# Kernel optimization log

Measured on AMD Instinct MI355X. Metric: run time of the kernel, lower is better.

Reference implementation:

```python
import jax, jax.numpy as jnp
import numpy as np
from jax.scipy.special import logsumexp

G, H, L, N, K = 2000, 128, 10, 4096, 10
TAU, LC, LA, EPS = 0.1, 1.0, 0.5, 1e-6

def _lin_init(k, fi, fo):
    return jax.random.normal(k, (fi, fo), jnp.float32) / np.sqrt(fi)

def setup_inputs():
    key = jax.random.key(0)
    ks = jax.random.split(key, 12)
    return {
        'wt_x': jax.random.normal(ks[0], (N, G), jnp.float32),
        'ko_x': jax.random.normal(ks[1], (N, G), jnp.float32),
        'wt_labels': jax.random.randint(ks[2], (N,), 0, K, dtype=jnp.int32),
        'ko_labels': jax.random.randint(ks[3], (N,), 0, K, dtype=jnp.int32),
        'enc_w1': _lin_init(ks[4], G, H), 'enc_b1': jnp.zeros((H,)),
        'enc_g': jnp.ones((H,)), 'enc_be': jnp.zeros((H,)),
        'enc_w2': _lin_init(ks[5], H, L), 'enc_b2': jnp.zeros((L,)),
        'kap_w1': _lin_init(ks[6], G, H), 'kap_b1': jnp.zeros((H,)),
        'kap_g': jnp.ones((H,)), 'kap_be': jnp.zeros((H,)),
        'kap_w2': _lin_init(ks[7], H, 1), 'kap_b2': jnp.zeros((1,)),
        'dec_w1': _lin_init(ks[8], L, H), 'dec_b1': jnp.zeros((H,)),
        'dec_g': jnp.ones((H,)), 'dec_be': jnp.zeros((H,)),
        'dec_w2': _lin_init(ks[9], H, G), 'dec_b2': jnp.zeros((G,)),
    }

def _mlp(x, w1, b1, g, be, w2, b2):
    # Linear -> LayerNorm -> ReLU -> Linear (dropout_prob=0)
    h = x @ w1 + b1
    m = h.mean(-1, keepdims=True)
    v = ((h - m) ** 2).mean(-1, keepdims=True)
    h = (h - m) / jnp.sqrt(v + 1e-5) * g + be
    return jax.nn.relu(h) @ w2 + b2

def _contrastive(z_wt, z_ko, y_wt, y_ko):
    S = (z_wt @ z_ko.T) / TAU  # [Nwt, Nko], unit-norm z so |S| <= 1/tau
    total = jnp.float32(0.0)
    n_shared = jnp.float32(0.0)
    for c in range(K):  # fixed small class count
        mwt = (y_wt == c).astype(S.dtype)
        mko = (y_ko == c).astype(S.dtype)
        n_wt, n_ko = mwt.sum(), mko.sum()
        valid = (n_wt > 0) & (n_ko > 0)
        nw, nk = jnp.maximum(n_wt, 1.0), jnp.maximum(n_ko, 1.0)
        # mean_{i in c, j in c} (LSE_i - S_ij) over ko columns of class c
        lse_r = logsumexp(jnp.where(mko[None, :] > 0, S, -1e4), axis=1)
        l1 = jnp.sum(mwt * (lse_r - (S @ mko) / nk)) / nw
        lse_c = logsumexp(jnp.where(mwt[:, None] > 0, S, -1e4), axis=0)
        l2 = jnp.sum(mko * (lse_c - (mwt @ S) / nw)) / nk
        total = total + jnp.where(valid, 0.5 * (l1 + l2), 0.0)
        n_shared = n_shared + valid.astype(S.dtype)
    return jnp.where(n_shared > 0, total / jnp.maximum(n_shared, 1.0), 0.0)

def _alignment(z, y):
    ones = jnp.ones(z.shape[0], z.dtype)
    counts = jax.ops.segment_sum(ones, y, num_segments=K)
    mu_c = jax.ops.segment_sum(z, y, num_segments=K) / jnp.maximum(counts, 1.0)[:, None]
    dev = z - mu_c[y]
    per_class = jax.ops.segment_sum(jnp.sum(dev ** 2, axis=1), y, num_segments=K) / jnp.maximum(counts, 1.0)
    present = counts > 0
    return jnp.sum(jnp.where(present, per_class, 0.0)) / jnp.maximum(jnp.sum(present.astype(z.dtype)), 1.0)

def reference(wt_x, ko_x, enc_w1, enc_b1, enc_g, enc_be, enc_w2, enc_b2, kap_w1, kap_b1, kap_g, kap_be, kap_w2, kap_b2, dec_w1, dec_b1, dec_g, dec_be, dec_w2, dec_b2, wt_labels, ko_labels):
    def encode(x):
        mu = _mlp(x, enc_w1, enc_b1, enc_g, enc_be, enc_w2, enc_b2)
        mu = mu / jnp.maximum(jnp.linalg.norm(mu, axis=1, keepdims=True), 1e-12)
        kappa = jax.nn.softplus(_mlp(x, kap_w1, kap_b1, kap_g, kap_be, kap_w2, kap_b2)) + EPS
        return mu, kappa
    wt_mu, wt_kappa = encode(wt_x)
    ko_mu, ko_kappa = encode(ko_x)
    wt_z, ko_z = wt_mu, ko_mu  # eval mode: z = mu (deterministic)
    wt_rec = _mlp(wt_z, dec_w1, dec_b1, dec_g, dec_be, dec_w2, dec_b2)
    ko_rec = _mlp(ko_z, dec_w1, dec_b1, dec_g, dec_be, dec_w2, dec_b2)
    recon = jnp.mean((wt_rec - wt_x) ** 2) + jnp.mean((ko_rec - ko_x) ** 2)
    kl = (wt_kappa.mean() + ko_kappa.mean()) * 0.01
    contrast = _contrastive(wt_z, ko_z, wt_labels, ko_labels)
    align = _alignment(jnp.concatenate([wt_z, ko_z], 0), jnp.concatenate([wt_labels, ko_labels], 0))
    return recon + kl + LC * contrast + LA * align
```

## Files before the change

kernel.cpp:

```cpp
#include <hip/hip_runtime.h>
#include <math.h>

typedef __attribute__((ext_vector_type(8))) __bf16 bf16x8;
typedef __attribute__((ext_vector_type(4))) float f32x4;

#define GL2LDS_(gptr, lptr) \
    __builtin_amdgcn_global_load_lds((const __attribute__((address_space(1))) void*)(gptr), \
                                     (__attribute__((address_space(3))) void*)(lptr), 16, 0, 0)

#define OFF_NWT   0
#define OFF_NKO   10
#define OFF_L1    20
#define OFF_L2    30
#define OFF_REC   162
#define IOFF_WTOFF 192
#define IOFF_KOOFF 204
#define IOFF_WTCTR 216
#define ACC_FLOATS 256

#define WT_OFF    256
#define WTLO_OFF  (WT_OFF + 262144)
#define H_OFF     (WTLO_OFF + 262144)
#define Z_OFF     (H_OFF + 2097152)
#define KAP_OFF   (Z_OFF + 81920)
#define HREST_OFF (KAP_OFF + 8192)
#define HPART     2097152

__global__ __launch_bounds__(256) void pack_w_kernel(const float* __restrict__ enc_w1,
                                                     const float* __restrict__ kap_w1,
                                                     __bf16* __restrict__ WThi)
{
    __shared__ float tile[64][65];
    int kt = blockIdx.x & 31;
    int ct = blockIdx.x >> 5;
    int k0 = kt * 64, c0 = ct * 64;
    int t = threadIdx.x;
    int lr = t >> 6, lc = t & 63;
#pragma unroll
    for (int i = 0; i < 16; ++i) {
        int k = k0 + lr + 4 * i;
        int c = c0 + lc;
        float v = 0.f;
        if (k < 2000) v = (c < 128) ? enc_w1[(size_t)k * 128 + c]
                                    : kap_w1[(size_t)k * 128 + (c - 128)];
        tile[lc][lr + 4 * i] = v;
    }
    __syncthreads();
#pragma unroll
    for (int i = 0; i < 16; ++i) {
        int c = c0 + lr + 4 * i;
        int k = k0 + lc;
        WThi[(size_t)c * 2048 + k] = (__bf16)tile[lr + 4 * i][lc];
    }
}

__global__ __launch_bounds__(256) void pack_dw2_kernel(const float* __restrict__ dw2,
                                                       __bf16* __restrict__ BThi)
{
    __shared__ float tile[64][129];
    int j0 = blockIdx.x * 64;
    int t = threadIdx.x;
#pragma unroll
    for (int i = 0; i < 32; ++i) {
        int idx = i * 256 + t;
        int c = idx >> 6, jj = idx & 63;
        int j = j0 + jj;
        tile[jj][c] = (j < 2000) ? dw2[(size_t)c * 2000 + j] : 0.f;
    }
    __syncthreads();
#pragma unroll
    for (int i = 0; i < 32; ++i) {
        int idx = i * 256 + t;
        int jj = idx >> 7, c = idx & 127;
        BThi[(size_t)(j0 + jj) * 128 + c] = (__bf16)tile[jj][c];
    }
}

__global__ void counts_kernel(const int* __restrict__ wtl, const int* __restrict__ kol,
                              float* __restrict__ acc)
{
    __shared__ int cw[10], ck[10];
    int t = threadIdx.x;
    if (t < 10) { cw[t] = 0; ck[t] = 0; }
    __syncthreads();
    for (int i = t; i < 4096; i += 1024) {
        atomicAdd(&cw[wtl[i]], 1);
        atomicAdd(&ck[kol[i]], 1);
    }
    __syncthreads();
    if (t < 10) { acc[OFF_NWT + t] = (float)cw[t]; acc[OFF_NKO + t] = (float)ck[t]; }
    if (t == 0) {
        int* ai = (int*)acc;
        int aw = 0, ak = 0;
        for (int c = 0; c < 10; ++c) {
            ai[IOFF_WTOFF + c] = aw; aw += cw[c];
            ai[IOFF_KOOFF + c] = ak; ak += ck[c];
        }
        ai[IOFF_WTOFF + 10] = aw;
        ai[IOFF_KOOFF + 10] = ak;
    }
}

__global__ __launch_bounds__(512) void gemm1_kernel(const float* __restrict__ wt_x,
                                                    const float* __restrict__ ko_x,
                                                    const __bf16* __restrict__ WThi,
                                                    float* __restrict__ Hb,
                                                    float* __restrict__ Hrest,
                                                    int nkc)
{
    __shared__ short Bs[2][2][4096];
    int t = threadIdx.x;
    int widx = t >> 6, lane = t & 63;
    int wm = widx >> 1, wn = widx & 1;
    int b = blockIdx.x;
    int mt = b & 63, strip = (b >> 6) & 1, kc = b >> 7;
    int R0 = mt * 128;
    int cb = strip * 128;
    int kchunk = 2048 / nkc;
    int kbase = kc * kchunk;
    int kleft = 2000 - kbase;
    int nsteps = (kleft < kchunk) ? ((kleft + 31) >> 5) : (kchunk >> 5);
    int ntiles = (nsteps + 1) >> 1;

    const float* xb = (R0 < 4096) ? (wt_x + (size_t)R0 * 2000)
                                  : (ko_x + (size_t)(R0 - 4096) * 2000);
    int ar = wm * 32 + (lane & 15);
    const float* xrow0 = xb + (size_t)ar * 2000 + kbase;
    const float* xrow1 = xrow0 + (size_t)16 * 2000;
    int kboff = (lane >> 4) * 8;

    int col0 = t >> 2;
    int s0   = (t & 3) ^ ((col0 >> 1) & 3);
    size_t boff = (size_t)(cb + col0) * 2048 + kbase + s0 * 8;
    const __bf16* bsrcH = WThi + boff;

#define STAGEB_(buf, tl) do { \
    int st_ = (tl) * 2; \
    GL2LDS_(bsrcH + (size_t)st_ * 32,       &Bs[buf][0][t * 8]); \
    GL2LDS_(bsrcH + (size_t)(st_ + 1) * 32, &Bs[buf][1][t * 8]); } while (0)

    f32x4 acc00, acc01, acc02, acc03;
    f32x4 acc10, acc11, acc12, acc13;
#pragma unroll
    for (int r = 0; r < 4; ++r) {
        acc00[r]=0.f; acc01[r]=0.f; acc02[r]=0.f; acc03[r]=0.f;
        acc10[r]=0.f; acc11[r]=0.f; acc12[r]=0.f; acc13[r]=0.f;
    }

    float4 aA00, aA01, aA10, aA11, aA20, aA21, aA30, aA31;
    float4 aB00, aB01, aB10, aB11, aB20, aB21, aB30, aB31;

#define GLOADA_(step, a00, a01, a10, a11) do { \
    int k0_ = (step) * 32; \
    int k_ = k0_ + kboff; \
    if (kbase + k0_ <= 1952) { \
        a00 = *(const float4*)(xrow0 + k_); \
        a01 = *(const float4*)(xrow0 + k_ + 4); \
        a10 = *(const float4*)(xrow1 + k_); \
        a11 = *(const float4*)(xrow1 + k_ + 4); \
    } else { \
        float t0_[8], t1_[8]; \
        _Pragma("unroll") \
        for (int j = 0; j < 8; ++j) { \
            int kk = kbase + k_ + j; \
            t0_[j] = (kk < 2000) ? xrow0[k_ + j] : 0.f; \
            t1_[j] = (kk < 2000) ? xrow1[k_ + j] : 0.f; } \
        a00 = make_float4(t0_[0], t0_[1], t0_[2], t0_[3]); \
        a01 = make_float4(t0_[4], t0_[5], t0_[6], t0_[7]); \
        a10 = make_float4(t1_[0], t1_[1], t1_[2], t1_[3]); \
        a11 = make_float4(t1_[4], t1_[5], t1_[6], t1_[7]); } } while (0)

#define CONVH_(a0, a1, ahi) do { \
    float av_[8] = {a0.x, a0.y, a0.z, a0.w, a1.x, a1.y, a1.z, a1.w}; \
    _Pragma("unroll") \
    for (int j = 0; j < 8; ++j) ahi[j] = (__bf16)av_[j]; } while (0)

#define MFMAH_(buf, half, ahi0, ahi1) do { \
    _Pragma("unroll") \
    for (int nf = 0; nf < 4; ++nf) { \
        bf16x8 bhf = *(const bf16x8*)&Bs[buf][half][(ubase + nf * 64) * 8]; \
        f32x4* p0 = (nf == 0) ? &acc00 : (nf == 1) ? &acc01 : (nf == 2) ? &acc02 : &acc03; \
        f32x4* p1 = (nf == 0) ? &acc10 : (nf == 1) ? &acc11 : (nf == 2) ? &acc12 : &acc13; \
        *p0 = __builtin_amdgcn_mfma_f32_16x16x32_bf16(ahi0, bhf, *p0, 0, 0, 0); \
        *p1 = __builtin_amdgcn_mfma_f32_16x16x32_bf16(ahi1, bhf, *p1, 0, 0, 0); } } while (0)

    STAGEB_(0, 0);
    GLOADA_(0, aA00, aA01, aA10, aA11);
    GLOADA_(1, aA20, aA21, aA30, aA31);
    if (1 < ntiles) {
        GLOADA_(2, aB00, aB01, aB10, aB11);
        GLOADA_(3, aB20, aB21, aB30, aB31);
    }
    __syncthreads();

    int cpr = lane & 15;
    int pph = (lane >> 4) ^ ((cpr >> 1) & 3);
    int ubase = (wn * 64 + cpr) * 4 + pph;

    int half_iters = (ntiles + 1) >> 1;
    for (int it = 0; it < half_iters; ++it) {
        int tl = it * 2;
        {
            if (tl + 1 < ntiles) STAGEB_(1, tl + 1);
            bf16x8 h00, h01, h10, h11;
            CONVH_(aA00, aA01, h00); CONVH_(aA10, aA11, h01);
            CONVH_(aA20, aA21, h10); CONVH_(aA30, aA31, h11);
            if (tl + 2 < ntiles) {
                GLOADA_(2*(tl+2),   aA00, aA01, aA10, aA11);
                GLOADA_(2*(tl+2)+1, aA20, aA21, aA30, aA31);
            }
            MFMAH_(0, 0, h00, h01);
            MFMAH_(0, 1, h10, h11);
            __syncthreads();
        }
        if (tl + 1 < ntiles) {
            if (tl + 2 < ntiles) STAGEB_(0, tl + 2);
            bf16x8 h00, h01, h10, h11;
            CONVH_(aB00, aB01, h00); CONVH_(aB10, aB11, h01);
            CONVH_(aB20, aB21, h10); CONVH_(aB30, aB31, h11);
            if (tl + 3 < ntiles) {
                GLOADA_(2*(tl+3),   aB00, aB01, aB10, aB11);
                GLOADA_(2*(tl+3)+1, aB20, aB21, aB30, aB31);
            }
            MFMAH_(1, 0, h00, h01);
            MFMAH_(1, 1, h10, h11);
            __syncthreads();
        }
    }

    float* Hq = (kc == 0) ? Hb : (Hrest + (size_t)(kc - 1) * HPART);
#pragma unroll
    for (int r = 0; r < 4; ++r) {
        int row0 = R0 + wm * 32 + (lane >> 4) * 4 + r;
        size_t base0 = (size_t)row0 * 256 + cb + wn * 64 + (lane & 15);
        Hq[base0]      = acc00[r];
        Hq[base0 + 16] = acc01[r];
        Hq[base0 + 32] = acc02[r];
        Hq[base0 + 48] = acc03[r];
        size_t base1 = base0 + (size_t)16 * 256;
        Hq[base1]      = acc10[r];
        Hq[base1 + 16] = acc11[r];
        Hq[base1 + 32] = acc12[r];
        Hq[base1 + 48] = acc13[r];
    }
#undef STAGEB_
#undef GLOADA_
#undef CONVH_
#undef MFMAH_
}

__global__ __launch_bounds__(128) void stage2_kernel(const float* __restrict__ Hb,
    const float* __restrict__ Hrest, int nkc,
    const float* __restrict__ enc_b1, const float* __restrict__ enc_g, const float* __restrict__ enc_be,
    const float* __restrict__ enc_w2, const float* __restrict__ enc_b2,
    const float* __restrict__ kap_b1, const float* __restrict__ kap_g, const float* __restrict__ kap_be,
    const float* __restrict__ kap_w2, const float* __restrict__ kap_b2,
    const float* __restrict__ dw1, const float* __restrict__ db1,
    const float* __restrict__ dg,  const float* __restrict__ dbe,
    float* __restrict__ Z, float* __restrict__ Kap,
    __bf16* __restrict__ Ahi)
{
    __shared__ float sh[128];
    __shared__ float shz[10];
    __shared__ float dred[2], dvar[2];
    int row  = blockIdx.x;
    int wave = threadIdx.x >> 6;
    int lane = threadIdx.x & 63;
    size_t hoff = (size_t)row * 256 + wave * 128;
    const float* hb  = Hb + hoff;
    const float* b1 = wave ? kap_b1 : enc_b1;
    const float* gg = wave ? kap_g  : enc_g;
    const float* bb = wave ? kap_be : enc_be;

    float h0 = hb[lane]      + b1[lane];
    float h1 = hb[lane + 64] + b1[lane + 64];
    for (int j = 0; j + 1 < nkc; ++j) {
        const float* hr = Hrest + (size_t)j * HPART + hoff;
        h0 += hr[lane];
        h1 += hr[lane + 64];
    }
    float s = h0 + h1;
#pragma unroll
    for (int o = 32; o > 0; o >>= 1) s += __shfl_xor(s, o, 64);
    float m = s * (1.f / 128.f);
    float d0 = h0 - m, d1 = h1 - m;
    float v = d0 * d0 + d1 * d1;
#pragma unroll
    for (int o = 32; o > 0; o >>= 1) v += __shfl_xor(v, o, 64);
    v *= (1.f / 128.f);
    float sc = 1.f / sqrtf(v + 1e-5f);
    float r0 = fmaxf(fmaf(d0 * sc, gg[lane],      bb[lane]),      0.f);
    float r1 = fmaxf(fmaf(d1 * sc, gg[lane + 64], bb[lane + 64]), 0.f);

    if (wave == 0) { sh[lane] = r0; sh[lane + 64] = r1; }
    __syncthreads();

    if (wave == 0) {
        float mu = 0.f;
        if (lane < 10) {
            mu = enc_b2[lane];
            for (int c = 0; c < 128; ++c) mu = fmaf(sh[c], enc_w2[c * 10 + lane], mu);
        }
        float n2 = mu * mu;
#pragma unroll
        for (int o = 8; o > 0; o >>= 1) n2 += __shfl_xor(n2, o, 16);
        float inv = 1.f / fmaxf(sqrtf(n2), 1e-12f);
        if (lane < 10) {
            float zv = mu * inv;
            Z[(size_t)row * 10 + lane] = zv;
            shz[lane] = zv;
        }
    } else {
        float p = r0 * kap_w2[lane] + r1 * kap_w2[lane + 64];
#pragma unroll
        for (int o = 32; o > 0; o >>= 1) p += __shfl_xor(p, o, 64);
        if (lane == 0) {
            float x = p + kap_b2[0];
            float sp = (x > 20.f) ? x : log1pf(expf(x));
            Kap[row] = sp + 1e-6f;
        }
    }
    __syncthreads();

    {
        float z[10];
#pragma unroll
        for (int d = 0; d < 10; ++d) z[d] = shz[d];
        int c = threadIdx.x;
        float h = db1[c];
#pragma unroll
        for (int d = 0; d < 10; ++d) h = fmaf(z[d], dw1[d * 128 + c], h);
        float s2 = h;
#pragma unroll
        for (int o = 32; o > 0; o >>= 1) s2 += __shfl_xor(s2, o, 64);
        if (lane == 0) dred[wave] = s2;
        __syncthreads();
        float m2 = (dred[0] + dred[1]) * (1.f / 128.f);
        float dd = h - m2;
        float v2 = dd * dd;
#pragma unroll
        for (int o = 32; o > 0; o >>= 1) v2 += __shfl_xor(v2, o, 64);
        if (lane == 0) dvar[wave] = v2;
        __syncthreads();
        float var = (dvar[0] + dvar[1]) * (1.f / 128.f);
        float sc2 = 1.f / sqrtf(var + 1e-5f);
        float a = fmaxf(fmaf(dd * sc2, dg[c], dbe[c]), 0.f);
        Ahi[(size_t)row * 128 + c] = (__bf16)a;
    }
}

__global__ __launch_bounds__(256) void scatter_align_kernel(const float* __restrict__ Z,
                                                            const int* __restrict__ wtl,
                                                            const int* __restrict__ kol,
                                                            const float* __restrict__ Kap,
                                                            float* __restrict__ acc,
                                                            float* __restrict__ ZcWT,
                                                            float* __restrict__ ZcKO,
                                                            float* __restrict__ Part)
{
    __shared__ int lcnt[20];
    __shared__ int lbase[20];
    __shared__ float cL[10], qL[10], sL[100], ks;
    int t = threadIdx.x;
    if (t < 20) lcnt[t] = 0;
    if (t < 10) { cL[t] = 0.f; qL[t] = 0.f; }
    if (t >= 20 && t < 120) sL[t - 20] = 0.f;
    if (t == 120) ks = 0.f;
    __syncthreads();
    int row = blockIdx.x * 256 + t;
    int side = row >= 4096;
    int r = side ? row - 4096 : row;
    int c = side ? kol[r] : wtl[r];
    int key = side * 10 + c;
    int myrank = atomicAdd(&lcnt[key], 1);
    float zz[10]; float q = 0.f;
    const float* zr = Z + (size_t)row * 10;
#pragma unroll
    for (int d = 0; d < 10; ++d) { zz[d] = zr[d]; q = fmaf(zz[d], zz[d], q); }
    atomicAdd(&cL[c], 1.f);
    atomicAdd(&qL[c], q);
#pragma unroll
    for (int d = 0; d < 10; ++d) atomicAdd(&sL[c * 10 + d], zz[d]);
    atomicAdd(&ks, Kap[row]);
    __syncthreads();
    int* ai = (int*)acc;
    if (t < 20 && lcnt[t] > 0)
        lbase[t] = atomicAdd(&ai[IOFF_WTCTR + t], lcnt[t]);
    __syncthreads();
    int off = side ? ai[IOFF_KOOFF + c] : ai[IOFF_WTOFF + c];
    int slot = off + lbase[key] + myrank;
    float* dst = side ? ZcKO : ZcWT;
#pragma unroll
    for (int d = 0; d < 10; ++d) dst[d * 4096 + slot] = zz[d];
    float* pb = Part + (size_t)blockIdx.x * 128;
    if (t < 10)  { pb[t] = cL[t]; pb[10 + t] = qL[t]; }
    if (t < 100) pb[20 + t] = sL[t];
    if (t == 0)  pb[120] = ks;
}

__global__ __launch_bounds__(512, 4) void dec_gemm_kernel(
    const __bf16* __restrict__ Ahi,
    const __bf16* __restrict__ BThi,
    const float* __restrict__ wt_x, const float* __restrict__ ko_x,
    const float* __restrict__ db2, float* __restrict__ acc)
{
    __shared__ short BsH[2][8192];
    __shared__ float rs[8];
    int t = threadIdx.x;
    int widx = t >> 6, lane = t & 63;
    int wm = widx >> 2, wn = widx & 3;
    int R0 = (blockIdx.x >> 1) * 32;
    int T0 = (blockIdx.x & 1) * 16;
    const float* xbase = (R0 < 4096) ? wt_x : ko_x;
    int xr0 = ((R0 < 4096) ? R0 : R0 - 4096) + wm * 16 + (lane >> 4) * 4;

    size_t abase = (size_t)(R0 + wm * 16 + (lane & 15)) * 128 + (lane >> 4) * 8;
    bf16x8 ah0 = *(const bf16x8*)(Ahi + abase);
    bf16x8 ah1 = *(const bf16x8*)(Ahi + abase + 32);
    bf16x8 ah2 = *(const bf16x8*)(Ahi + abase + 64);
    bf16x8 ah3 = *(const bf16x8*)(Ahi + abase + 96);

    int g0c = t >> 4,         g0s = t & 15;
    int g1c = (t + 512) >> 4, g1s = t & 15;
    int u0 = g0c * 16 + (g0s ^ (g0c & 7));
    int u1 = g1c * 16 + (g1s ^ (g1c & 7));

    int col_local = wn * 16 + (lane & 15);
    int cl7 = col_local & 7;
    int rb = col_local * 16;
    int sb = lane >> 4;

    uint4 hA0, hA1, hB0, hB1;

#define GLOADB_(tile, h0, h1) do { \
    size_t gb = (size_t)(tile) * 8192; \
    h0 = *(const uint4*)(BThi + gb + (size_t)t * 8); \
    h1 = *(const uint4*)(BThi + gb + (size_t)(t + 512) * 8); } while (0)

#define DSWRITE_(buf, h0, h1) do { \
    *(uint4*)&BsH[buf][u0 * 8] = h0; \
    *(uint4*)&BsH[buf][u1 * 8] = h1; } while (0)

#define COMPUTE_(buf, tile) do { \
    int un0 = rb + ((sb +  0) ^ cl7); \
    int un1 = rb + ((sb +  4) ^ cl7); \
    int un2 = rb + ((sb +  8) ^ cl7); \
    int un3 = rb + ((sb + 12) ^ cl7); \
    bf16x8 bh0 = *(const bf16x8*)&BsH[buf][un0 * 8]; \
    bf16x8 bh1 = *(const bf16x8*)&BsH[buf][un1 * 8]; \
    bf16x8 bh2 = *(const bf16x8*)&BsH[buf][un2 * 8]; \
    bf16x8 bh3 = *(const bf16x8*)&BsH[buf][un3 * 8]; \
    f32x4 a4; \
    _Pragma("unroll") \
    for (int r = 0; r < 4; ++r) a4[r] = 0.f; \
    a4 = __builtin_amdgcn_mfma_f32_16x16x32_bf16(ah0, bh0, a4, 0, 0, 0); \
    a4 = __builtin_amdgcn_mfma_f32_16x16x32_bf16(ah1, bh1, a4, 0, 0, 0); \
    a4 = __builtin_amdgcn_mfma_f32_16x16x32_bf16(ah2, bh2, a4, 0, 0, 0); \
    a4 = __builtin_amdgcn_mfma_f32_16x16x32_bf16(ah3, bh3, a4, 0, 0, 0); \
    int col = (tile) * 64 + col_local; \
    if (col < 2000) { \
        float bb = db2[col]; \
        _Pragma("unroll") \
        for (int r = 0; r < 4; ++r) { \
            float xv = xbase[(size_t)(xr0 + r) * 2000 + col]; \
            float e = a4[r] + bb - xv; \
            rsum = fmaf(e, e, rsum); \
        } } } while (0)

    float rsum = 0.f;
    GLOADB_(T0 + 0, hA0, hA1);
    GLOADB_(T0 + 1, hB0, hB1);
    DSWRITE_(0, hA0, hA1);
    __syncthreads();

    for (int it = 0; it < 8; ++it) {
        int lt = it * 2;
        {
            if (lt + 2 < 16) GLOADB_(T0 + lt + 2, hA0, hA1);
            DSWRITE_(1, hB0, hB1);
            COMPUTE_(0, T0 + lt);
            __syncthreads();
        }
        {
            if (lt + 3 < 16) GLOADB_(T0 + lt + 3, hB0, hB1);
            if (lt + 2 < 16) DSWRITE_(0, hA0, hA1);
            COMPUTE_(1, T0 + lt + 1);
            __syncthreads();
        }
    }

#pragma unroll
    for (int o = 32; o > 0; o >>= 1) rsum += __shfl_xor(rsum, o, 64);
    if (lane == 0) rs[widx] = rsum;
    __syncthreads();
    if (t == 0) {
        float s = 0.f;
#pragma unroll
        for (int w = 0; w < 8; ++w) s += rs[w];
        atomicAdd(&acc[OFF_REC], s);
    }
#undef GLOADB_
#undef DSWRITE_
#undef COMPUTE_
}

#define MAXNB 768
__global__ __launch_bounds__(256) void contrast_kernel(const float* __restrict__ ZcWT,
                                                       const float* __restrict__ ZcKO,
                                                       float* __restrict__ acc)
{
    __shared__ float zb[MAXNB * 12];
    __shared__ float bsum[4];
    int b = blockIdx.x;
    int cs = b / 3, sub = b - cs * 3;
    int c = cs >> 1, side = cs & 1;
    const int* ai = (const int*)acc;
    int aStart = side ? ai[IOFF_KOOFF + c]     : ai[IOFF_WTOFF + c];
    int aEnd   = side ? ai[IOFF_KOOFF + c + 1] : ai[IOFF_WTOFF + c + 1];
    int bStart = side ? ai[IOFF_WTOFF + c]     : ai[IOFF_KOOFF + c];
    int bEnd   = side ? ai[IOFF_WTOFF + c + 1] : ai[IOFF_KOOFF + c + 1];
    int na = aEnd - aStart;
    int nb = bEnd - bStart;
    if (nb > MAXNB) nb = MAXNB;
    const float* ZA = side ? ZcKO : ZcWT;
    const float* ZB = side ? ZcWT : ZcKO;
    int t = threadIdx.x;

    for (int u = t; u < nb; u += 256) {
#pragma unroll
        for (int d = 0; d < 10; ++d) zb[u * 12 + d] = ZB[d * 4096 + bStart + u];
    }
    __syncthreads();

    int chunk = (na + 2) / 3;
    int r0 = sub * chunk;
    int rcnt = na - r0; if (rcnt > chunk) rcnt = chunk;

    float wsum = 0.f;
    bool waveActive = (nb > 0) && ((t & ~63) < rcnt);
    if (waveActive) {
        bool valid = t < rcnt;
        int ar = aStart + (valid ? (r0 + t) : 0);
        float za[10];
#pragma unroll
        for (int d = 0; d < 10; ++d) za[d] = ZA[d * 4096 + ar];
        float se = 0.f, ss = 0.f;
        for (int u = 0; u < nb; ++u) {
            const float* zp = &zb[u * 12];
            float s = 0.f;
#pragma unroll
            for (int d = 0; d < 10; ++d) s = fmaf(za[d], zp[d], s);
            s *= 10.f;
            se += __expf(s - 10.f);
            ss += s;
        }
        if (valid) wsum = (10.f + __logf(se)) - ss / (float)nb;
    }
#pragma unroll
    for (int o = 32; o > 0; o >>= 1) wsum += __shfl_xor(wsum, o, 64);
    if ((t & 63) == 0) bsum[t >> 6] = wsum;
    __syncthreads();
    if (t == 0) {
        float s = bsum[0] + bsum[1] + bsum[2] + bsum[3];
        if (s != 0.f || nb > 0)
            atomicAdd(&acc[(side ? OFF_L2 : OFF_L1) + c], s);
    }
}

__global__ void finalize_kernel(const float* __restrict__ Part,
                                const float* __restrict__ acc,
                                float* __restrict__ out)
{
    __shared__ float red[121];
    int t = threadIdx.x;
    if (t < 120) {
        float s = 0.f;
        for (int b = 0; b < 32; ++b) s += Part[(size_t)b * 128 + t];
        red[t] = s;
    } else if (t == 120) {
        float s = 0.f;
        for (int b = 0; b < 32; ++b) s += Part[(size_t)b * 128 + 120];
        red[120] = s;
    }
    __syncthreads();
    if (t == 0) {
        float total = 0.f, nsh = 0.f;
        for (int c = 0; c < 10; ++c) {
            float nw = acc[OFF_NWT + c], nk = acc[OFF_NKO + c];
            if (nw > 0.5f && nk > 0.5f) {
                float l1 = acc[OFF_L1 + c] / nw;
                float l2 = acc[OFF_L2 + c] / nk;
                total += 0.5f * (l1 + l2);
                nsh += 1.f;
            }
        }
        float contrast = (nsh > 0.f) ? total / nsh : 0.f;
        float ap = 0.f, np_ = 0.f;
        for (int c = 0; c < 10; ++c) {
            float cn = red[c];
            if (cn > 0.5f) {
                float mu2 = 0.f;
                for (int d = 0; d < 10; ++d) {
                    float mm = red[20 + c * 10 + d] / cn;
                    mu2 = fmaf(mm, mm, mu2);
                }
                ap += red[10 + c] / cn - mu2;
                np_ += 1.f;
            }
        }
        float align = (np_ > 0.f) ? ap / np_ : 0.f;
        float kl = 0.01f * red[120] * (1.f / 4096.f);
        float recon = acc[OFF_REC] * (1.f / 8192000.f);
        out[0] = recon + kl + 1.0f * contrast + 0.5f * align;
    }
}

extern "C" void kernel_launch(void* const* d_in, const int* in_sizes, int n_in,
                              void* d_out, int out_size, void* d_ws, size_t ws_size,
                              hipStream_t stream)
{
    const float* wt_x   = (const float*)d_in[0];
    const float* ko_x   = (const float*)d_in[1];
    const int*   wtl    = (const int*)d_in[2];
    const int*   kol    = (const int*)d_in[3];
    const float* enc_w1 = (const float*)d_in[4];
    const float* enc_b1 = (const float*)d_in[5];
    const float* enc_g  = (const float*)d_in[6];
    const float* enc_be = (const float*)d_in[7];
    const float* enc_w2 = (const float*)d_in[8];
    const float* enc_b2 = (const float*)d_in[9];
    const float* kap_w1 = (const float*)d_in[10];
    const float* kap_b1 = (const float*)d_in[11];
    const float* kap_g  = (const float*)d_in[12];
    const float* kap_be = (const float*)d_in[13];
    const float* kap_w2 = (const float*)d_in[14];
    const float* kap_b2 = (const float*)d_in[15];
    const float* dw1    = (const float*)d_in[16];
    const float* db1    = (const float*)d_in[17];
    const float* dg     = (const float*)d_in[18];
    const float* dbe    = (const float*)d_in[19];
    const float* dw2    = (const float*)d_in[20];
    const float* db2    = (const float*)d_in[21];

    float* ws  = (float*)d_ws;
    float* acc = ws;
    __bf16* WThi = (__bf16*)(ws + WT_OFF);
    float* Hb    = ws + H_OFF;
    float* Zb    = ws + Z_OFF;
    float* Kap   = ws + KAP_OFF;
    float* Hrest = ws + HREST_OFF;

    const size_t TAIL = 2 * 524288 + 2 * 131072 + 2 * 40960 + 4096;
    size_t need4 = (size_t)(HREST_OFF + 3 * HPART + TAIL) * sizeof(float);
    int nkc = (ws_size >= need4) ? 4 : 2;

    float* tail = ws + HREST_OFF + (size_t)(nkc - 1) * HPART;
    __bf16* Ahi  = (__bf16*)tail;
    __bf16* BThi = (__bf16*)(tail + 1048576);
    float* ZcKO = tail + 1048576 + 262144;
    float* ZcWT = ZcKO + 40960;
    float* Part = ZcWT + 40960;

    hipMemsetAsync(acc, 0, ACC_FLOATS * sizeof(float), stream);
    pack_w_kernel<<<128, 256, 0, stream>>>(enc_w1, kap_w1, WThi);
    counts_kernel<<<1, 1024, 0, stream>>>(wtl, kol, acc);
    gemm1_kernel<<<128 * nkc, 512, 0, stream>>>(wt_x, ko_x, WThi, Hb, Hrest, nkc);
    stage2_kernel<<<8192, 128, 0, stream>>>(Hb, Hrest, nkc, enc_b1, enc_g, enc_be, enc_w2, enc_b2,
                                            kap_b1, kap_g, kap_be, kap_w2, kap_b2,
                                            dw1, db1, dg, dbe, Zb, Kap, Ahi);
    pack_dw2_kernel<<<32, 256, 0, stream>>>(dw2, BThi);
    scatter_align_kernel<<<32, 256, 0, stream>>>(Zb, wtl, kol, Kap, acc, ZcWT, ZcKO, Part);
    contrast_kernel<<<60, 256, 0, stream>>>(ZcWT, ZcKO, acc);
    dec_gemm_kernel<<<512, 512, 0, stream>>>(Ahi, BThi, wt_x, ko_x, db2, acc);
    finalize_kernel<<<1, 128, 0, stream>>>(Part, acc, (float*)d_out);
}
```

Baseline: 150.4 us.

## Stage B tiles via registers and use LDS-only waitcnt barriers in GEMM loops

```diff
diff --git a/kernel.cpp b/kernel.cpp
--- a/kernel.cpp
+++ b/kernel.cpp
@@ -4,9 +4,10 @@
 typedef __attribute__((ext_vector_type(8))) __bf16 bf16x8;
 typedef __attribute__((ext_vector_type(4))) float f32x4;
 
-#define GL2LDS_(gptr, lptr) \
-    __builtin_amdgcn_global_load_lds((const __attribute__((address_space(1))) void*)(gptr), \
-                                     (__attribute__((address_space(3))) void*)(lptr), 16, 0, 0)
+#define LGKB_() do { \
+    asm volatile("s_waitcnt lgkmcnt(0)" ::: "memory"); \
+    __builtin_amdgcn_s_barrier(); \
+    __builtin_amdgcn_sched_barrier(0); } while (0)
 
 #define OFF_NWT   0
 #define OFF_NKO   10
@@ -134,10 +135,14 @@
     size_t boff = (size_t)(cb + col0) * 2048 + kbase + s0 * 8;
     const __bf16* bsrcH = WThi + boff;
 
-#define STAGEB_(buf, tl) do { \
+#define GLOADB_(tl, b0, b1) do { \
     int st_ = (tl) * 2; \
-    GL2LDS_(bsrcH + (size_t)st_ * 32,       &Bs[buf][0][t * 8]); \
-    GL2LDS_(bsrcH + (size_t)(st_ + 1) * 32, &Bs[buf][1][t * 8]); } while (0)
+    b0 = *(const uint4*)(bsrcH + (size_t)st_ * 32); \
+    b1 = *(const uint4*)(bsrcH + (size_t)(st_ + 1) * 32); } while (0)
+
+#define DSWRITE_(buf, b0, b1) do { \
+    *(uint4*)&Bs[buf][0][t * 8] = b0; \
+    *(uint4*)&Bs[buf][1][t * 8] = b1; } while (0)
 
     f32x4 acc00, acc01, acc02, acc03;
     f32x4 acc10, acc11, acc12, acc13;
@@ -147,6 +152,7 @@
         acc10[r]=0.f; acc11[r]=0.f; acc12[r]=0.f; acc13[r]=0.f;
     }
 
+    uint4 bA0, bA1, bB0, bB1;
     float4 aA00, aA01, aA10, aA11, aA20, aA21, aA30, aA31;
     float4 aB00, aB01, aB10, aB11, aB20, aB21, aB30, aB31;
 
@@ -184,14 +190,16 @@
         *p0 = __builtin_amdgcn_mfma_f32_16x16x32_bf16(ahi0, bhf, *p0, 0, 0, 0); \
         *p1 = __builtin_amdgcn_mfma_f32_16x16x32_bf16(ahi1, bhf, *p1, 0, 0, 0); } } while (0)
 
-    STAGEB_(0, 0);
+    GLOADB_(0, bA0, bA1);
     GLOADA_(0, aA00, aA01, aA10, aA11);
     GLOADA_(1, aA20, aA21, aA30, aA31);
+    GLOADB_(1, bB0, bB1);
     if (1 < ntiles) {
         GLOADA_(2, aB00, aB01, aB10, aB11);
         GLOADA_(3, aB20, aB21, aB30, aB31);
     }
-    __syncthreads();
+    DSWRITE_(0, bA0, bA1);
+    LGKB_();
 
     int cpr = lane & 15;
     int pph = (lane >> 4) ^ ((cpr >> 1) & 3);
@@ -201,7 +209,8 @@
     for (int it = 0; it < half_iters; ++it) {
         int tl = it * 2;
         {
-            if (tl + 1 < ntiles) STAGEB_(1, tl + 1);
+            if (tl + 2 < ntiles) GLOADB_(tl + 2, bA0, bA1);
+            if (tl + 1 < ntiles) DSWRITE_(1, bB0, bB1);
             bf16x8 h00, h01, h10, h11;
             CONVH_(aA00, aA01, h00); CONVH_(aA10, aA11, h01);
             CONVH_(aA20, aA21, h10); CONVH_(aA30, aA31, h11);
@@ -211,10 +220,11 @@
             }
             MFMAH_(0, 0, h00, h01);
             MFMAH_(0, 1, h10, h11);
-            __syncthreads();
+            LGKB_();
         }
         if (tl + 1 < ntiles) {
-            if (tl + 2 < ntiles) STAGEB_(0, tl + 2);
+            if (tl + 3 < ntiles) GLOADB_(tl + 3, bB0, bB1);
+            if (tl + 2 < ntiles) DSWRITE_(0, bA0, bA1);
             bf16x8 h00, h01, h10, h11;
             CONVH_(aB00, aB01, h00); CONVH_(aB10, aB11, h01);
             CONVH_(aB20, aB21, h10); CONVH_(aB30, aB31, h11);
@@ -224,7 +234,7 @@
             }
             MFMAH_(1, 0, h00, h01);
             MFMAH_(1, 1, h10, h11);
-            __syncthreads();
+            LGKB_();
         }
     }
 
@@ -243,7 +253,8 @@
         Hq[base1 + 32] = acc12[r];
         Hq[base1 + 48] = acc13[r];
     }
-#undef STAGEB_
+#undef GLOADB_
+#undef DSWRITE_
 #undef GLOADA_
 #undef CONVH_
 #undef MFMAH_
@@ -471,7 +482,7 @@
     GLOADB_(T0 + 0, hA0, hA1);
     GLOADB_(T0 + 1, hB0, hB1);
     DSWRITE_(0, hA0, hA1);
-    __syncthreads();
+    LGKB_();
 
     for (int it = 0; it < 8; ++it) {
         int lt = it * 2;
@@ -479,13 +490,13 @@
             if (lt + 2 < 16) GLOADB_(T0 + lt + 2, hA0, hA1);
             DSWRITE_(1, hB0, hB1);
             COMPUTE_(0, T0 + lt);
-            __syncthreads();
+            LGKB_();
         }
         {
             if (lt + 3 < 16) GLOADB_(T0 + lt + 3, hB0, hB1);
             if (lt + 2 < 16) DSWRITE_(0, hA0, hA1);
             COMPUTE_(1, T0 + lt + 1);
-            __syncthreads();
+            LGKB_();
         }
     }
 
```

Measured after the change: 149.6 us. About the same (-0.5%).
